# Optimization experiments

Measured on AMD Instinct MI355X. Metric: run time of the kernel, lower is better.

The kernel has to match this reference:

```python
import jax, jax.numpy as jnp
import numpy as np

N_NODES = 100000
N_EDGES = 1600000
D_FEAT = 48


def setup_inputs() -> dict:
    key = jax.random.key(0)
    k1, k2, k3, k4 = jax.random.split(key, 4)
    rows = jax.random.randint(k1, (N_EDGES,), 0, N_NODES, dtype=jnp.int32)
    cols = jax.random.randint(k2, (N_EDGES,), 0, N_NODES, dtype=jnp.int32)
    # normalized adjacency values (positive, like D^-1/2 A D^-1/2 entries)
    vals = jax.random.uniform(k3, (N_EDGES,), dtype=jnp.float32)
    embeds = jax.random.normal(k4, (N_NODES, D_FEAT), dtype=jnp.float32)
    return {"rows": rows, "cols": cols, "vals": vals, "embeds": embeds}


def reference(rows, cols, vals, embeds):
    # torch.spmm(adj, embeds) with adj in COO form:
    # out[i] = sum_{e : rows[e]==i} vals[e] * embeds[cols[e]]
    msgs = vals[:, None] * embeds[cols]          # [E, D] gather + scale
    out = jax.ops.segment_sum(msgs, rows, num_segments=embeds.shape[0])  # [N, D]
    return out
```

## Files before the change

### kernel.cpp

```cpp
#include <hip/hip_runtime.h>


#define N_NODES 100000
#define D_FEAT 48
#define DQ (D_FEAT / 4)

#define BUCKET_BITS 7
#define BUCKET_NODES 128
#define N_BUCKETS ((N_NODES + BUCKET_NODES - 1) / BUCKET_NODES)
#define CAPB 2432

#define CHUNK 8192
#define P1_THREADS 1024
#define VPT (CHUNK / P1_THREADS / 4)

#define P2_THREADS 512
#define EPT2 ((CAPB + P2_THREADS - 1) / P2_THREADS)
#define NG (P2_THREADS / 12)

#define OVF_CAP 4096
#define EBF_UINT2 (N_NODES * DQ)

typedef float  fl32x4 __attribute__((ext_vector_type(4)));
typedef unsigned long long u64;

__device__ __forceinline__ unsigned short f2bf(float f) {
    unsigned u = __float_as_uint(f);
    return (unsigned short)((u + 0x7FFFu + ((u >> 16) & 1u)) >> 16);
}

__device__ __forceinline__ float4 bf2f4(uint2 h) {
    float4 m;
    m.x = __uint_as_float((h.x & 0xFFFFu) << 16);
    m.y = __uint_as_float(h.x & 0xFFFF0000u);
    m.z = __uint_as_float((h.y & 0xFFFFu) << 16);
    m.w = __uint_as_float(h.y & 0xFFFF0000u);
    return m;
}

__global__ __launch_bounds__(P1_THREADS) void partition_kernel(
        const int* __restrict__ rows, const int* __restrict__ cols,
        const float* __restrict__ vals, int* __restrict__ gcur,
        uint2* __restrict__ tmp, uint4* __restrict__ ovf, int* __restrict__ novf,
        const float* __restrict__ embeds, uint2* __restrict__ ebf,
        int n_edges) {
    __shared__ int counts[N_BUCKETS];
    __shared__ int cursor[N_BUCKETS];
    __shared__ int gpos[N_BUCKETS];

    int t = threadIdx.x;
    int base = blockIdx.x * CHUNK;
    int n = min(CHUNK, n_edges - base);
    int n4 = n >> 2;

    for (int i = t; i < N_BUCKETS; i += P1_THREADS) { counts[i] = 0; cursor[i] = 0; }
    __syncthreads();

    int      b[VPT * 4];
    unsigned key[VPT * 4];
    float    v[VPT * 4];
    const int4*   rows4 = reinterpret_cast<const int4*>(rows + base);
    const int4*   cols4 = reinterpret_cast<const int4*>(cols + base);
    const float4* vals4 = reinterpret_cast<const float4*>(vals + base);
#pragma unroll
    for (int k = 0; k < VPT; ++k) {
        int idx4 = k * P1_THREADS + t;
        bool ok = idx4 < n4;
        int4   r4 = ok ? rows4[idx4] : make_int4(0, 0, 0, 0);
        int4   c4 = ok ? cols4[idx4] : make_int4(0, 0, 0, 0);
        float4 v4 = ok ? vals4[idx4] : make_float4(0.f, 0.f, 0.f, 0.f);
        int rr[4] = {r4.x, r4.y, r4.z, r4.w};
        int cc[4] = {c4.x, c4.y, c4.z, c4.w};
        float vv[4] = {v4.x, v4.y, v4.z, v4.w};
#pragma unroll
        for (int j = 0; j < 4; ++j) {
            int i = k * 4 + j;
            b[i] = -1;
            if (ok) {
                b[i] = rr[j] >> BUCKET_BITS;
                key[i] = ((unsigned)(rr[j] & (BUCKET_NODES - 1)) << 17) | (unsigned)cc[j];
                v[i] = vv[j];
                atomicAdd(&counts[b[i]], 1);
            }
        }
    }

    if (ebf) {
        const float4* e4 = reinterpret_cast<const float4*>(embeds);
        int stride = gridDim.x * P1_THREADS;
        for (int i = blockIdx.x * P1_THREADS + t; i < EBF_UINT2; i += stride) {
            float4 f = e4[i];
            uint2 p;
            p.x = (unsigned)f2bf(f.x) | ((unsigned)f2bf(f.y) << 16);
            p.y = (unsigned)f2bf(f.z) | ((unsigned)f2bf(f.w) << 16);
            ebf[i] = p;
        }
    }
    __syncthreads();

    for (int i = t; i < N_BUCKETS; i += P1_THREADS)
        gpos[i] = (counts[i] > 0) ? atomicAdd(&gcur[i], counts[i]) : 0;
    __syncthreads();

#pragma unroll
    for (int i = 0; i < VPT * 4; ++i) {
        if (b[i] >= 0) {
            int p = atomicAdd(&cursor[b[i]], 1);
            int pos = gpos[b[i]] + p;
            if (pos < CAPB) {
                tmp[(size_t)b[i] * CAPB + pos] = make_uint2(key[i], __float_as_uint(v[i]));
            } else {
                int o = atomicAdd(novf, 1);
                if (o < OVF_CAP) {
                    unsigned rl = key[i] >> 17;
                    ovf[o] = make_uint4((unsigned)b[i] * BUCKET_NODES + rl,
                                        key[i] & 0x1FFFFu, __float_as_uint(v[i]), 0u);
                }
            }
        }
    }
}

#define ACCUM_OVF_TAIL(GATHER_EXPR)                                             \
    {                                                                           \
        int nov = min(*novf, OVF_CAP);                                          \
        if (nov > 0) {                                                          \
            __syncthreads();                                                    \
            int lo = bkt * BUCKET_NODES, hi = lo + BUCKET_NODES;                \
            for (int i = t; i < nov; i += P2_THREADS) {                         \
                uint4 en = ovf[i];                                              \
                int node = (int)en.x;                                           \
                if (node >= lo && node < hi && node < N_NODES) {                \
                    unsigned c = en.y;                                          \
                    float v = __uint_as_float(en.z);                            \
                    for (int qq = 0; qq < DQ; ++qq) {                           \
                        float4 m = GATHER_EXPR;                                 \
                        float* dst = out + (size_t)node * D_FEAT + qq * 4;      \
                        atomicAdd(dst + 0, v * m.x);                            \
                        atomicAdd(dst + 1, v * m.y);                            \
                        atomicAdd(dst + 2, v * m.z);                            \
                        atomicAdd(dst + 3, v * m.w);                            \
                    }                                                           \
                }                                                               \
            }                                                                   \
        }                                                                       \
    }

__global__ __launch_bounds__(P2_THREADS) void accum_bf16_kernel(
        const int* __restrict__ gcur, const uint2* __restrict__ tmp,
        const uint2* __restrict__ ebf, float* __restrict__ out,
        const int* __restrict__ novf, const uint4* __restrict__ ovf) {
    __shared__ uint2 sorted[CAPB];
    __shared__ int cnt[BUCKET_NODES];
    __shared__ int cur[BUCKET_NODES];
    __shared__ int roff[BUCKET_NODES + 1];
    __shared__ int ws2[2];

    int t = threadIdx.x;
    int lane = t & 63;
    int bkt = blockIdx.x;
    const uint2* bucket = tmp + (size_t)bkt * CAPB;
    int cntE = min(gcur[bkt], CAPB);

    if (t < BUCKET_NODES) cnt[t] = 0;
    __syncthreads();

    unsigned kcol[EPT2]; unsigned vbits[EPT2]; int erl[EPT2];
#pragma unroll
    for (int j = 0; j < EPT2; ++j) {
        int idx = t + j * P2_THREADS;
        erl[j] = -1;
        if (idx < cntE) {
            u64 pk8 = __builtin_nontemporal_load(
                reinterpret_cast<const u64*>(bucket) + idx);
            unsigned kx = (unsigned)pk8;
            erl[j] = (int)(kx >> 17);
            kcol[j] = kx & 0x1FFFFu;
            vbits[j] = (unsigned)(pk8 >> 32);
            atomicAdd(&cnt[erl[j]], 1);
        }
    }
    __syncthreads();

    int x = 0;
    if (t < BUCKET_NODES) {
        x = cnt[t];
#pragma unroll
        for (int d = 1; d < 64; d <<= 1) {
            int y = __shfl_up(x, d, 64);
            if (lane >= d) x += y;
        }
        if (lane == 63) ws2[t >> 6] = x;
    }
    __syncthreads();
    if (t == 0) { int a = ws2[0]; ws2[0] = 0; ws2[1] = a; }
    __syncthreads();
    if (t < BUCKET_NODES) {
        int incl = x + ws2[t >> 6];
        int st = incl - cnt[t];
        roff[t] = st; cur[t] = st;
    }
    if (t == 0) roff[BUCKET_NODES] = cntE;
    __syncthreads();

#pragma unroll
    for (int j = 0; j < EPT2; ++j) {
        if (erl[j] >= 0) {
            int pos = atomicAdd(&cur[erl[j]], 1);
            sorted[pos] = make_uint2(kcol[j], vbits[j]);
        }
    }
    __syncthreads();

    int g = t / 12, q = t - g * 12;
    if (g < NG) {
        const uint2* ebq = ebf + q;
        for (int rl = g; rl < BUCKET_NODES; rl += NG) {
            int e = roff[rl], e1 = roff[rl + 1];
            float4 a = make_float4(0.f, 0.f, 0.f, 0.f);
            for (; e + 3 < e1; e += 4) {
                uint2 p0 = sorted[e],     p1 = sorted[e + 1];
                uint2 p2 = sorted[e + 2], p3 = sorted[e + 3];
                uint2 h0 = ebq[p0.x * DQ];
                uint2 h1 = ebq[p1.x * DQ];
                uint2 h2 = ebq[p2.x * DQ];
                uint2 h3 = ebq[p3.x * DQ];
                float v0 = __uint_as_float(p0.y), v1 = __uint_as_float(p1.y);
                float v2 = __uint_as_float(p2.y), v3 = __uint_as_float(p3.y);
                float4 m0 = bf2f4(h0), m1 = bf2f4(h1);
                float4 m2 = bf2f4(h2), m3 = bf2f4(h3);
                a.x += v0 * m0.x; a.y += v0 * m0.y; a.z += v0 * m0.z; a.w += v0 * m0.w;
                a.x += v1 * m1.x; a.y += v1 * m1.y; a.z += v1 * m1.z; a.w += v1 * m1.w;
                a.x += v2 * m2.x; a.y += v2 * m2.y; a.z += v2 * m2.z; a.w += v2 * m2.w;
                a.x += v3 * m3.x; a.y += v3 * m3.y; a.z += v3 * m3.z; a.w += v3 * m3.w;
            }
            for (; e < e1; ++e) {
                uint2 p0 = sorted[e];
                float4 m0 = bf2f4(ebq[p0.x * DQ]);
                float v0 = __uint_as_float(p0.y);
                a.x += v0 * m0.x; a.y += v0 * m0.y; a.z += v0 * m0.z; a.w += v0 * m0.w;
            }
            int node = bkt * BUCKET_NODES + rl;
            if (node < N_NODES) {
                fl32x4 av = {a.x, a.y, a.z, a.w};
                __builtin_nontemporal_store(
                    av, reinterpret_cast<fl32x4*>(out + (size_t)node * D_FEAT) + q);
            }
        }
    }
    ACCUM_OVF_TAIL(bf2f4(ebf[c * DQ + qq]))
}

__global__ __launch_bounds__(P2_THREADS) void accum_f32_kernel(
        const int* __restrict__ gcur, const uint2* __restrict__ tmp,
        const float* __restrict__ embeds, float* __restrict__ out,
        const int* __restrict__ novf, const uint4* __restrict__ ovf) {
    __shared__ uint2 sorted[CAPB];
    __shared__ int cnt[BUCKET_NODES];
    __shared__ int cur[BUCKET_NODES];
    __shared__ int roff[BUCKET_NODES + 1];
    __shared__ int ws2[2];
    int t = threadIdx.x;
    int lane = t & 63;
    int bkt = blockIdx.x;
    const uint2* bucket = tmp + (size_t)bkt * CAPB;
    int cntE = min(gcur[bkt], CAPB);
    if (t < BUCKET_NODES) cnt[t] = 0;
    __syncthreads();
    unsigned kcol[EPT2]; unsigned vbits[EPT2]; int erl[EPT2];
#pragma unroll
    for (int j = 0; j < EPT2; ++j) {
        int idx = t + j * P2_THREADS;
        erl[j] = -1;
        if (idx < cntE) {
            uint2 pk = bucket[idx];
            erl[j] = (int)(pk.x >> 17);
            kcol[j] = pk.x & 0x1FFFFu;
            vbits[j] = pk.y;
            atomicAdd(&cnt[erl[j]], 1);
        }
    }
    __syncthreads();
    int x = 0;
    if (t < BUCKET_NODES) {
        x = cnt[t];
#pragma unroll
        for (int d = 1; d < 64; d <<= 1) {
            int y = __shfl_up(x, d, 64);
            if (lane >= d) x += y;
        }
        if (lane == 63) ws2[t >> 6] = x;
    }
    __syncthreads();
    if (t == 0) { int a = ws2[0]; ws2[0] = 0; ws2[1] = a; }
    __syncthreads();
    if (t < BUCKET_NODES) {
        int incl = x + ws2[t >> 6];
        int st = incl - cnt[t];
        roff[t] = st; cur[t] = st;
    }
    if (t == 0) roff[BUCKET_NODES] = cntE;
    __syncthreads();
#pragma unroll
    for (int j = 0; j < EPT2; ++j) {
        if (erl[j] >= 0) {
            int p = atomicAdd(&cur[erl[j]], 1);
            sorted[p] = make_uint2(kcol[j], vbits[j]);
        }
    }
    __syncthreads();
    int g = t / 12;
    int q = t - g * 12;
    if (g < NG) {
        for (int rl = g; rl < BUCKET_NODES; rl += NG) {
            int s = roff[rl], epos = roff[rl + 1];
            float4 a0 = make_float4(0.f, 0.f, 0.f, 0.f);
            int e = s;
            for (; e < epos; ++e) {
                uint2 p0 = sorted[e];
                float4 m0 = *(reinterpret_cast<const float4*>(embeds + p0.x * D_FEAT) + q);
                float v0 = __uint_as_float(p0.y);
                a0.x += v0 * m0.x; a0.y += v0 * m0.y; a0.z += v0 * m0.z; a0.w += v0 * m0.w;
            }
            int node = bkt * BUCKET_NODES + rl;
            if (node < N_NODES)
                *(reinterpret_cast<float4*>(out + (size_t)node * D_FEAT) + q) = a0;
        }
    }
    ACCUM_OVF_TAIL((*(reinterpret_cast<const float4*>(embeds + (size_t)c * D_FEAT) + qq)))
}

extern "C" void kernel_launch(void* const* d_in, const int* in_sizes, int n_in,
                              void* d_out, int out_size, void* d_ws, size_t ws_size,
                              hipStream_t stream) {
    const int*   rows   = (const int*)d_in[0];
    const int*   cols   = (const int*)d_in[1];
    const float* vals   = (const float*)d_in[2];
    const float* embeds = (const float*)d_in[3];
    float*       out    = (float*)d_out;
    int n_edges = in_sizes[0];

    const size_t TMP_OFF = 4096 + 65536;
    const size_t TMP_SZ  = (size_t)N_BUCKETS * CAPB * sizeof(uint2);
    const size_t EBF_OFF = TMP_OFF + TMP_SZ;
    const size_t EBF_SZ  = (size_t)EBF_UINT2 * sizeof(uint2);
    char* ws = (char*)d_ws;
    int*   gcur = (int*)(ws);
    int*   novf = (int*)(ws + 3200);
    uint4* ovf  = (uint4*)(ws + 4096);
    uint2* tmp  = (uint2*)(ws + TMP_OFF);
    uint2* ebf  = (uint2*)(ws + EBF_OFF);

    bool use_bf16 = ws_size >= EBF_OFF + EBF_SZ;

    hipMemsetAsync(ws, 0, 3264, stream);

    int p1_blocks = (n_edges + CHUNK - 1) / CHUNK;
    partition_kernel<<<p1_blocks, P1_THREADS, 0, stream>>>(
        rows, cols, vals, gcur, tmp, ovf, novf,
        embeds, use_bf16 ? ebf : (uint2*)nullptr, n_edges);

    if (use_bf16)
        accum_bf16_kernel<<<N_BUCKETS, P2_THREADS, 0, stream>>>(gcur, tmp, ebf, out, novf, ovf);
    else
        accum_f32_kernel<<<N_BUCKETS, P2_THREADS, 0, stream>>>(gcur, tmp, embeds, out, novf, ovf);
}
```

Before: 135.3 us.

## Stage partitioned edges in LDS by bucket for coalesced global writes

Each partition block now runs a block-wide prefix scan over its per-bucket edge counts. It places every edge into a bucket-sorted LDS staging area along with its precomputed global destination, then writes the staged entries to tmp in order. Consecutive threads therefore write to mostly contiguous addresses instead of scattering 8-byte stores randomly across buckets. The cost is about 100KB of extra LDS per block, one more barrier and an extra LDS round trip per edge.

```diff
diff --git a/kernel.cpp b/kernel.cpp
--- a/kernel.cpp
+++ b/kernel.cpp
@@ -45,15 +45,22 @@
         const float* __restrict__ embeds, uint2* __restrict__ ebf,
         int n_edges) {
     __shared__ int counts[N_BUCKETS];
+    __shared__ int starts[N_BUCKETS];
     __shared__ int cursor[N_BUCKETS];
-    __shared__ int gpos[N_BUCKETS];
+    __shared__ int adj[N_BUCKETS];
+    __shared__ int wtot[16];
+    __shared__ unsigned lkey[CHUNK];
+    __shared__ unsigned lval[CHUNK];
+    __shared__ int      ldst[CHUNK];
 
     int t = threadIdx.x;
+    int lane = t & 63;
+    int wid = t >> 6;
     int base = blockIdx.x * CHUNK;
     int n = min(CHUNK, n_edges - base);
     int n4 = n >> 2;
 
-    for (int i = t; i < N_BUCKETS; i += P1_THREADS) { counts[i] = 0; cursor[i] = 0; }
+    for (int i = t; i < N_BUCKETS; i += P1_THREADS) counts[i] = 0;
     __syncthreads();
 
     int      b[VPT * 4];
@@ -98,18 +105,46 @@
     }
     __syncthreads();
 
-    for (int i = t; i < N_BUCKETS; i += P1_THREADS)
-        gpos[i] = (counts[i] > 0) ? atomicAdd(&gcur[i], counts[i]) : 0;
+    int cnt_t = (t < N_BUCKETS) ? counts[t] : 0;
+    int x = cnt_t;
+#pragma unroll
+    for (int d = 1; d < 64; d <<= 1) {
+        int y = __shfl_up(x, d, 64);
+        if (lane >= d) x += y;
+    }
+    if (lane == 63) wtot[wid] = x;
+    __syncthreads();
+    if (t < 64) {
+        int w = (t < 16) ? wtot[t] : 0;
+        int xs = w;
+#pragma unroll
+        for (int d = 1; d < 16; d <<= 1) {
+            int y = __shfl_up(xs, d, 64);
+            if (lane >= d) xs += y;
+        }
+        if (t < 16) wtot[t] = xs - w;
+    }
+    __syncthreads();
+    if (t < N_BUCKETS) {
+        int excl = x - cnt_t + wtot[wid];
+        starts[t] = excl;
+        cursor[t] = excl;
+        int gp = (cnt_t > 0) ? atomicAdd(&gcur[t], cnt_t) : 0;
+        adj[t] = t * CAPB + gp - excl;
+    }
     __syncthreads();
 
 #pragma unroll
     for (int i = 0; i < VPT * 4; ++i) {
         if (b[i] >= 0) {
             int p = atomicAdd(&cursor[b[i]], 1);
-            int pos = gpos[b[i]] + p;
-            if (pos < CAPB) {
-                tmp[(size_t)b[i] * CAPB + pos] = make_uint2(key[i], __float_as_uint(v[i]));
+            int dest = adj[b[i]] + p;
+            if (dest < (b[i] + 1) * CAPB) {
+                lkey[p] = key[i];
+                lval[p] = __float_as_uint(v[i]);
+                ldst[p] = dest;
             } else {
+                ldst[p] = -1;
                 int o = atomicAdd(novf, 1);
                 if (o < OVF_CAP) {
                     unsigned rl = key[i] >> 17;
@@ -118,6 +153,14 @@
                 }
             }
         }
+    }
+    __syncthreads();
+
+    u64* tmp8 = reinterpret_cast<u64*>(tmp);
+    for (int i = t; i < n; i += P1_THREADS) {
+        int d = ldst[i];
+        if (d >= 0)
+            tmp8[d] = (u64)lkey[i] | ((u64)lval[i] << 32);
     }
 }
 
```

Result: no change. 133.7 us (-1.2%).

## Stage partitioned edges in LDS and write bucket runs coalesced

Applied to the files above, without the earlier changes.

The partition pass now does a block-wide prefix scan over bucket counts and scatters each edge into a shared-memory staging array ordered by bucket. A second loop then streams those contiguous runs to the global bucket arrays, so consecutive threads write consecutive addresses instead of scattering single 8-byte stores. Chunk size and block size are reduced so the staging buffers fit in LDS, which means more blocks and more global atomics on the bucket cursors. The extra scan and synchronisation add work per block.

```diff
diff --git a/kernel.cpp b/kernel.cpp
--- a/kernel.cpp
+++ b/kernel.cpp
@@ -10,8 +10,8 @@
 #define N_BUCKETS ((N_NODES + BUCKET_NODES - 1) / BUCKET_NODES)
 #define CAPB 2432
 
-#define CHUNK 8192
-#define P1_THREADS 1024
+#define CHUNK 2048
+#define P1_THREADS 512
 #define VPT (CHUNK / P1_THREADS / 4)
 
 #define P2_THREADS 512
@@ -44,16 +44,21 @@
         uint2* __restrict__ tmp, uint4* __restrict__ ovf, int* __restrict__ novf,
         const float* __restrict__ embeds, uint2* __restrict__ ebf,
         int n_edges) {
+    __shared__ u64            lkv[CHUNK];
+    __shared__ unsigned short lbkt[CHUNK];
     __shared__ int counts[N_BUCKETS];
     __shared__ int cursor[N_BUCKETS];
-    __shared__ int gpos[N_BUCKETS];
+    __shared__ int adj[N_BUCKETS];
+    __shared__ int wtot[P1_THREADS / 64];
 
     int t = threadIdx.x;
+    int lane = t & 63;
+    int wid = t >> 6;
     int base = blockIdx.x * CHUNK;
     int n = min(CHUNK, n_edges - base);
     int n4 = n >> 2;
 
-    for (int i = t; i < N_BUCKETS; i += P1_THREADS) { counts[i] = 0; cursor[i] = 0; }
+    for (int i = t; i < N_BUCKETS; i += P1_THREADS) counts[i] = 0;
     __syncthreads();
 
     int      b[VPT * 4];
@@ -98,25 +103,61 @@
     }
     __syncthreads();
 
-    for (int i = t; i < N_BUCKETS; i += P1_THREADS)
-        gpos[i] = (counts[i] > 0) ? atomicAdd(&gcur[i], counts[i]) : 0;
+    int c0 = 0, c1 = 0, s = 0;
+    if (t < N_BUCKETS / 2) {
+        c0 = counts[2 * t];
+        c1 = counts[2 * t + 1];
+        s = c0 + c1;
+    }
+    int x = s;
+#pragma unroll
+    for (int d = 1; d < 64; d <<= 1) {
+        int y = __shfl_up(x, d, 64);
+        if (lane >= d) x += y;
+    }
+    if (lane == 63) wtot[wid] = x;
+    __syncthreads();
+    if (t == 0) {
+        int run = 0;
+#pragma unroll
+        for (int i = 0; i < P1_THREADS / 64; ++i) { int a = wtot[i]; wtot[i] = run; run += a; }
+    }
+    __syncthreads();
+    if (t < N_BUCKETS / 2) {
+        int excl0 = wtot[wid] + x - s;
+        int b0 = 2 * t, b1 = 2 * t + 1;
+        cursor[b0] = excl0;
+        cursor[b1] = excl0 + c0;
+        int gp0 = (c0 > 0) ? atomicAdd(&gcur[b0], c0) : 0;
+        int gp1 = (c1 > 0) ? atomicAdd(&gcur[b1], c1) : 0;
+        adj[b0] = b0 * CAPB + gp0 - excl0;
+        adj[b1] = b1 * CAPB + gp1 - (excl0 + c0);
+    }
     __syncthreads();
 
 #pragma unroll
     for (int i = 0; i < VPT * 4; ++i) {
         if (b[i] >= 0) {
             int p = atomicAdd(&cursor[b[i]], 1);
-            int pos = gpos[b[i]] + p;
-            if (pos < CAPB) {
-                tmp[(size_t)b[i] * CAPB + pos] = make_uint2(key[i], __float_as_uint(v[i]));
-            } else {
-                int o = atomicAdd(novf, 1);
-                if (o < OVF_CAP) {
-                    unsigned rl = key[i] >> 17;
-                    ovf[o] = make_uint4((unsigned)b[i] * BUCKET_NODES + rl,
-                                        key[i] & 0x1FFFFu, __float_as_uint(v[i]), 0u);
-                }
-            }
+            lkv[p] = (u64)key[i] | ((u64)__float_as_uint(v[i]) << 32);
+            lbkt[p] = (unsigned short)b[i];
+        }
+    }
+    __syncthreads();
+
+    u64* tmp8 = reinterpret_cast<u64*>(tmp);
+    for (int i = t; i < n; i += P1_THREADS) {
+        int bb = lbkt[i];
+        int dest = adj[bb] + i;
+        if (dest < (bb + 1) * CAPB) {
+            tmp8[dest] = lkv[i];
+        } else {
+            u64 kv = lkv[i];
+            unsigned kk = (unsigned)kv;
+            int o = atomicAdd(novf, 1);
+            if (o < OVF_CAP)
+                ovf[o] = make_uint4((unsigned)bb * BUCKET_NODES + (kk >> 17),
+                                    kk & 0x1FFFFu, (unsigned)(kv >> 32), 0u);
         }
     }
 }
```

Result: slower. 156.5 us (+15.7%).
